# Kernel optimization log

Hardware: AMD Instinct MI355X
Metric: run time of the kernel (lower is better)

## Reference

```python
import jax, jax.numpy as jnp
import numpy as np

B, DS, DM = 4, 64, 4096
NE, S = 1024, 2048


def setup_inputs() -> dict:
    key = jax.random.key(0)
    ks = jax.random.split(key, 9)
    std = 0.02
    return {
        "state": jax.random.normal(ks[0], (B, DS, DM), jnp.float32),
        "evicted_tokens": jax.random.normal(ks[1], (B, NE, DM), jnp.float32),
        "current_tokens": jax.random.normal(ks[2], (B, S, DM), jnp.float32),
        "W_key": std * jax.random.normal(ks[3], (DS, DM), jnp.float32),
        "W_beta_w": std * jax.random.normal(ks[4], (DS, DM), jnp.float32),
        "W_beta_b": jnp.zeros((DS,), jnp.float32),
        "W_query": std * jax.random.normal(ks[5], (DS, DM), jnp.float32),
        "gate_w": std * jax.random.normal(ks[6], (1, DM), jnp.float32),
        "gate_b": jnp.full((1,), -2.0, jnp.float32),  # gate_bias init
    }


def reference(state, evicted_tokens, current_tokens, W_key, W_beta_w, W_beta_b,
              W_query, gate_w, gate_b):
    # ---- compress: fold evicted tokens into SSM state ----
    # keys: [B, NE, DS]; softmax over the token axis (dim=1)
    keys = jnp.einsum('bnd,sd->bns', evicted_tokens, W_key)
    write_weights = jax.nn.softmax(keys, axis=1)
    # update: [B, DS, DM] = write_weights^T @ evicted_tokens
    update = jnp.einsum('bns,bnd->bsd', write_weights, evicted_tokens)
    summary = evicted_tokens.mean(axis=1)  # [B, DM]
    beta = jax.nn.sigmoid(summary @ W_beta_w.T + W_beta_b)  # [B, DS]
    new_state = beta[:, :, None] * state + update  # [B, DS, DM]
    # ---- query: gated linear-attention readout ----
    q = jnp.einsum('bld,sd->bls', current_tokens, W_query)  # [B, S, DS]
    retrieved = jnp.einsum('bls,bsd->bld', q, new_state)    # [B, S, DM]
    gate = jax.nn.sigmoid(current_tokens @ gate_w.T + gate_b)  # [B, S, 1]
    return gate * retrieved
```

## Files before the change

kernel.cpp:

```cpp
#include <hip/hip_runtime.h>

#define DM 4096
#define DSZ 64
#define NE 1024
#define SQ 2048
#define NB 4

typedef __attribute__((ext_vector_type(8))) short bf16x8;
typedef __attribute__((ext_vector_type(4))) float f32x4;

__device__ __forceinline__ unsigned f2bf(float f) {
  union { float f; unsigned u; } v; v.f = f;
  return (v.u + 0x7fffu + ((v.u >> 16) & 1u)) >> 16;
}
__device__ __forceinline__ unsigned pack2(float lo, float hi) {
  return f2bf(lo) | (f2bf(hi) << 16);
}

__launch_bounds__(256)
__global__ void k_keys(const float* __restrict__ ev, const float* __restrict__ Wk,
                       float* __restrict__ keys_part) {
  __shared__ __align__(16) unsigned short As[64][72];
  __shared__ __align__(16) unsigned short Bs[64][72];
  const int bid = blockIdx.x;
  const int ks = bid & 7, mt = (bid >> 3) & 15, b = bid >> 7;
  const int n0 = mt * 64;
  const int t = threadIdx.x;
  const int w = t >> 6, m15 = t & 15, quad = (t & 63) >> 4;
  const int rowS = t >> 2, seg = (t & 3) * 16;

  f32x4 acc[4];
#pragma unroll
  for (int i = 0; i < 4; ++i) acc[i] = (f32x4){0.f, 0.f, 0.f, 0.f};

  const float* ap = ev + ((size_t)(b * NE + n0 + rowS)) * DM + ks * 512 + seg;
  const float* bp = Wk + (size_t)rowS * DM + ks * 512 + seg;

  for (int ch = 0; ch < 8; ++ch) {
    float4 a0 = *(const float4*)(ap);
    float4 a1 = *(const float4*)(ap + 4);
    float4 a2 = *(const float4*)(ap + 8);
    float4 a3 = *(const float4*)(ap + 12);
    float4 b0 = *(const float4*)(bp);
    float4 b1 = *(const float4*)(bp + 4);
    float4 b2 = *(const float4*)(bp + 8);
    float4 b3 = *(const float4*)(bp + 12);
    uint4 pa0 = { pack2(a0.x,a0.y), pack2(a0.z,a0.w), pack2(a1.x,a1.y), pack2(a1.z,a1.w) };
    uint4 pa1 = { pack2(a2.x,a2.y), pack2(a2.z,a2.w), pack2(a3.x,a3.y), pack2(a3.z,a3.w) };
    uint4 pb0 = { pack2(b0.x,b0.y), pack2(b0.z,b0.w), pack2(b1.x,b1.y), pack2(b1.z,b1.w) };
    uint4 pb1 = { pack2(b2.x,b2.y), pack2(b2.z,b2.w), pack2(b3.x,b3.y), pack2(b3.z,b3.w) };
    *(uint4*)&As[rowS][seg]     = pa0;
    *(uint4*)&As[rowS][seg + 8] = pa1;
    *(uint4*)&Bs[rowS][seg]     = pb0;
    *(uint4*)&Bs[rowS][seg + 8] = pb1;
    __syncthreads();
#pragma unroll
    for (int kk = 0; kk < 2; ++kk) {
      bf16x8 af = *(const bf16x8*)&As[w * 16 + m15][kk * 32 + quad * 8];
#pragma unroll
      for (int tn = 0; tn < 4; ++tn) {
        bf16x8 bfr = *(const bf16x8*)&Bs[tn * 16 + m15][kk * 32 + quad * 8];
        acc[tn] = __builtin_amdgcn_mfma_f32_16x16x32_bf16(af, bfr, acc[tn], 0, 0, 0);
      }
    }
    __syncthreads();
    ap += 64; bp += 64;
  }
  const int n = n0 + w * 16 + quad * 4;
#pragma unroll
  for (int tn = 0; tn < 4; ++tn) {
    const int s = tn * 16 + m15;
    float4 v = { acc[tn][0], acc[tn][1], acc[tn][2], acc[tn][3] };
    *(float4*)&keys_part[(size_t)ks * (NB * DSZ * NE) + ((size_t)(b * DSZ + s)) * NE + n] = v;
  }
}

__launch_bounds__(256)
__global__ void k_sum(const float* __restrict__ ev, float* __restrict__ summary) {
  __shared__ float red[256];
  const int bid = blockIdx.x;
  const int b = bid >> 7, rem = bid & 127;
  const int d0 = (rem >> 1) * 64, half = rem & 1;
  const int t = threadIdx.x;
  const int dl = t & 63, g = t >> 6;
  float acc = 0.f;
  const float* p = ev + ((size_t)(b * NE + half * 512 + g * 128)) * DM + d0 + dl;
  for (int i = 0; i < 128; ++i) { acc += *p; p += DM; }
  red[t] = acc;
  __syncthreads();
  if (t < 64) {
    float tot = red[t] + red[t + 64] + red[t + 128] + red[t + 192];
    atomicAdd(&summary[b * DM + d0 + t], tot * (1.f / 1024.f));
  }
}

__launch_bounds__(256)
__global__ void k_beta(const float* __restrict__ summary, const float* __restrict__ Wbw,
                       const float* __restrict__ Wbb, float* __restrict__ beta) {
  __shared__ float red[256];
  const int b = blockIdx.x >> 6, s = blockIdx.x & 63;
  const int t = threadIdx.x;
  const float* sp = summary + b * DM + t * 16;
  const float* wp = Wbw + (size_t)s * DM + t * 16;
  float acc = 0.f;
#pragma unroll
  for (int j = 0; j < 4; ++j) {
    float4 a  = *(const float4*)(sp + j * 4);
    float4 w4 = *(const float4*)(wp + j * 4);
    acc += a.x * w4.x + a.y * w4.y + a.z * w4.z + a.w * w4.w;
  }
  red[t] = acc;
  __syncthreads();
  for (int off = 128; off > 0; off >>= 1) {
    if (t < off) red[t] += red[t + off];
    __syncthreads();
  }
  if (t == 0) {
    float x = red[0] + Wbb[s];
    beta[b * DSZ + s] = 1.f / (1.f + expf(-x));
  }
}

__launch_bounds__(256)
__global__ void k_softmax(const float* __restrict__ keys_part, unsigned short* __restrict__ ww_t) {
  __shared__ float red[256];
  const int b = blockIdx.x >> 6, s = blockIdx.x & 63;
  const int t = threadIdx.x;
  const size_t base = ((size_t)(b * DSZ + s)) * NE + t * 4;
  float4 k = {0.f, 0.f, 0.f, 0.f};
#pragma unroll
  for (int sl = 0; sl < 8; ++sl) {
    float4 p = *(const float4*)&keys_part[(size_t)sl * (NB * DSZ * NE) + base];
    k.x += p.x; k.y += p.y; k.z += p.z; k.w += p.w;
  }
  float m = fmaxf(fmaxf(k.x, k.y), fmaxf(k.z, k.w));
  red[t] = m;
  __syncthreads();
  for (int off = 128; off > 0; off >>= 1) {
    if (t < off) red[t] = fmaxf(red[t], red[t + off]);
    __syncthreads();
  }
  const float M = red[0];
  __syncthreads();
  float4 e = { expf(k.x - M), expf(k.y - M), expf(k.z - M), expf(k.w - M) };
  red[t] = e.x + e.y + e.z + e.w;
  __syncthreads();
  for (int off = 128; off > 0; off >>= 1) {
    if (t < off) red[t] += red[t + off];
    __syncthreads();
  }
  const float inv = 1.f / red[0];
  ushort4 o = { (unsigned short)f2bf(e.x * inv), (unsigned short)f2bf(e.y * inv),
                (unsigned short)f2bf(e.z * inv), (unsigned short)f2bf(e.w * inv) };
  *(ushort4*)&ww_t[((size_t)(b * DSZ + s)) * NE + t * 4] = o;
}

__launch_bounds__(256)
__global__ void k_update(const float* __restrict__ ev, const float* __restrict__ state,
                         const float* __restrict__ beta, const unsigned short* __restrict__ ww_t,
                         unsigned short* __restrict__ ns_t) {
  __shared__ __align__(16) unsigned short Aw[64][72];
  __shared__ __align__(16) unsigned short Bt[64][72];
  const int bid = blockIdx.x;
  const int dt = bid & 63, b = bid >> 6;
  const int d0 = dt * 64;
  const int t = threadIdx.x;
  const int w = t >> 6, m15 = t & 15, quad = (t & 63) >> 4;
  const int rowS = t >> 2, seg = (t & 3) * 16;
  const int npair = (t & 31) * 2, dseg = (t >> 5) * 8;

  f32x4 acc[4];
#pragma unroll
  for (int i = 0; i < 4; ++i) acc[i] = (f32x4){0.f, 0.f, 0.f, 0.f};

  for (int ch = 0; ch < 16; ++ch) {
    const int nch = ch * 64;
    const uint4* wsrc = (const uint4*)&ww_t[((size_t)(b * DSZ + rowS)) * NE + nch + seg];
    uint4 wa = wsrc[0], wb = wsrc[1];
    const float* e0 = ev + ((size_t)(b * NE + nch + npair)) * DM + d0 + dseg;
    const float* e1 = e0 + DM;
    float4 r00 = *(const float4*)(e0);
    float4 r01 = *(const float4*)(e0 + 4);
    float4 r10 = *(const float4*)(e1);
    float4 r11 = *(const float4*)(e1 + 4);
    *(uint4*)&Aw[rowS][seg]     = wa;
    *(uint4*)&Aw[rowS][seg + 8] = wb;
    *(unsigned*)&Bt[dseg + 0][npair] = pack2(r00.x, r10.x);
    *(unsigned*)&Bt[dseg + 1][npair] = pack2(r00.y, r10.y);
    *(unsigned*)&Bt[dseg + 2][npair] = pack2(r00.z, r10.z);
    *(unsigned*)&Bt[dseg + 3][npair] = pack2(r00.w, r10.w);
    *(unsigned*)&Bt[dseg + 4][npair] = pack2(r01.x, r11.x);
    *(unsigned*)&Bt[dseg + 5][npair] = pack2(r01.y, r11.y);
    *(unsigned*)&Bt[dseg + 6][npair] = pack2(r01.z, r11.z);
    *(unsigned*)&Bt[dseg + 7][npair] = pack2(r01.w, r11.w);
    __syncthreads();
#pragma unroll
    for (int kk = 0; kk < 2; ++kk) {
      bf16x8 af = *(const bf16x8*)&Aw[w * 16 + m15][kk * 32 + quad * 8];
#pragma unroll
      for (int tn = 0; tn < 4; ++tn) {
        bf16x8 bfr = *(const bf16x8*)&Bt[tn * 16 + m15][kk * 32 + quad * 8];
        acc[tn] = __builtin_amdgcn_mfma_f32_16x16x32_bf16(af, bfr, acc[tn], 0, 0, 0);
      }
    }
    __syncthreads();
  }
  const int sbase = w * 16 + quad * 4;
#pragma unroll
  for (int tn = 0; tn < 4; ++tn) {
    const int d = d0 + tn * 16 + m15;
    float v[4];
#pragma unroll
    for (int r = 0; r < 4; ++r) {
      const int s = sbase + r;
      v[r] = beta[b * DSZ + s] * state[((size_t)(b * DSZ + s)) * DM + d] + acc[tn][r];
    }
    ushort4 o = { (unsigned short)f2bf(v[0]), (unsigned short)f2bf(v[1]),
                  (unsigned short)f2bf(v[2]), (unsigned short)f2bf(v[3]) };
    *(ushort4*)&ns_t[((size_t)(b * DM + d)) * DSZ + sbase] = o;
  }
}

__launch_bounds__(256)
__global__ void k_q(const float* __restrict__ cur, const float* __restrict__ Wq,
                    const float* __restrict__ gate_w,
                    float* __restrict__ q_part, float* __restrict__ gate_acc) {
  __shared__ __align__(16) unsigned short As[64][72];
  __shared__ __align__(16) unsigned short Bs[64][72];
  __shared__ float gw[64];
  __shared__ float gred[256];
  const int bid = blockIdx.x;
  const int ks = bid & 3, mt = (bid >> 2) & 31, b = bid >> 7;
  const int l0 = mt * 64;
  const int t = threadIdx.x;
  const int w = t >> 6, m15 = t & 15, quad = (t & 63) >> 4;
  const int rowS = t >> 2, seg = (t & 3) * 16;

  f32x4 acc[4];
#pragma unroll
  for (int i = 0; i < 4; ++i) acc[i] = (f32x4){0.f, 0.f, 0.f, 0.f};
  float gpart = 0.f;

  const float* ap = cur + ((size_t)(b * SQ + l0 + rowS)) * DM + ks * 1024 + seg;
  const float* bp = Wq + (size_t)rowS * DM + ks * 1024 + seg;
  const float* gp = gate_w + ks * 1024;

  for (int ch = 0; ch < 16; ++ch) {
    float4 a0 = *(const float4*)(ap);
    float4 a1 = *(const float4*)(ap + 4);
    float4 a2 = *(const float4*)(ap + 8);
    float4 a3 = *(const float4*)(ap + 12);
    float4 b0 = *(const float4*)(bp);
    float4 b1 = *(const float4*)(bp + 4);
    float4 b2 = *(const float4*)(bp + 8);
    float4 b3 = *(const float4*)(bp + 12);
    if (t < 16) *(float4*)&gw[t * 4] = *(const float4*)(gp + ch * 64 + t * 4);
    uint4 pa0 = { pack2(a0.x,a0.y), pack2(a0.z,a0.w), pack2(a1.x,a1.y), pack2(a1.z,a1.w) };
    uint4 pa1 = { pack2(a2.x,a2.y), pack2(a2.z,a2.w), pack2(a3.x,a3.y), pack2(a3.z,a3.w) };
    uint4 pb0 = { pack2(b0.x,b0.y), pack2(b0.z,b0.w), pack2(b1.x,b1.y), pack2(b1.z,b1.w) };
    uint4 pb1 = { pack2(b2.x,b2.y), pack2(b2.z,b2.w), pack2(b3.x,b3.y), pack2(b3.z,b3.w) };
    *(uint4*)&As[rowS][seg]     = pa0;
    *(uint4*)&As[rowS][seg + 8] = pa1;
    *(uint4*)&Bs[rowS][seg]     = pb0;
    *(uint4*)&Bs[rowS][seg + 8] = pb1;
    __syncthreads();
    {
      const float* g = &gw[seg];
      gpart += a0.x*g[0]  + a0.y*g[1]  + a0.z*g[2]  + a0.w*g[3]
             + a1.x*g[4]  + a1.y*g[5]  + a1.z*g[6]  + a1.w*g[7]
             + a2.x*g[8]  + a2.y*g[9]  + a2.z*g[10] + a2.w*g[11]
             + a3.x*g[12] + a3.y*g[13] + a3.z*g[14] + a3.w*g[15];
    }
#pragma unroll
    for (int kk = 0; kk < 2; ++kk) {
      bf16x8 af = *(const bf16x8*)&As[w * 16 + m15][kk * 32 + quad * 8];
#pragma unroll
      for (int tn = 0; tn < 4; ++tn) {
        bf16x8 bfr = *(const bf16x8*)&Bs[tn * 16 + m15][kk * 32 + quad * 8];
        acc[tn] = __builtin_amdgcn_mfma_f32_16x16x32_bf16(af, bfr, acc[tn], 0, 0, 0);
      }
    }
    __syncthreads();
    ap += 64; bp += 64;
  }
  const int lrow = l0 + w * 16 + quad * 4;
#pragma unroll
  for (int tn = 0; tn < 4; ++tn) {
#pragma unroll
    for (int r = 0; r < 4; ++r) {
      q_part[(size_t)ks * (NB * SQ * DSZ) + ((size_t)(b * SQ + lrow + r)) * DSZ + tn * 16 + m15] =
          acc[tn][r];
    }
  }
  gred[t] = gpart;
  __syncthreads();
  if (t < 64) {
    float tot = gred[4 * t] + gred[4 * t + 1] + gred[4 * t + 2] + gred[4 * t + 3];
    atomicAdd(&gate_acc[b * SQ + l0 + t], tot);
  }
}

__launch_bounds__(256)
__global__ void k_qcvt(const float* __restrict__ q_part, unsigned short* __restrict__ qbf) {
  const int i = (blockIdx.x * 256 + threadIdx.x) * 4;
  const int SL = NB * SQ * DSZ;
  float4 v0 = *(const float4*)&q_part[i];
  float4 v1 = *(const float4*)&q_part[i + SL];
  float4 v2 = *(const float4*)&q_part[i + 2 * SL];
  float4 v3 = *(const float4*)&q_part[i + 3 * SL];
  float x = v0.x + v1.x + v2.x + v3.x;
  float y = v0.y + v1.y + v2.y + v3.y;
  float z = v0.z + v1.z + v2.z + v3.z;
  float u = v0.w + v1.w + v2.w + v3.w;
  ushort4 o = { (unsigned short)f2bf(x), (unsigned short)f2bf(y),
                (unsigned short)f2bf(z), (unsigned short)f2bf(u) };
  *(ushort4*)&qbf[i] = o;
}

__launch_bounds__(256)
__global__ void k_out(const unsigned short* __restrict__ qbf, const unsigned short* __restrict__ ns_t,
                      const float* __restrict__ gate_acc, const float* __restrict__ gate_b,
                      float* __restrict__ out) {
  const int bid = blockIdx.x;
  const int dt = bid & 63, lt = (bid >> 6) & 31, b = bid >> 11;
  const int d0 = dt * 64, l0 = lt * 64;
  const int t = threadIdx.x;
  const int w = t >> 6, m15 = t & 15, quad = (t & 63) >> 4;
  const int la = l0 + w * 16 + m15;
  f32x4 acc[4];
#pragma unroll
  for (int i = 0; i < 4; ++i) acc[i] = (f32x4){0.f, 0.f, 0.f, 0.f};
#pragma unroll
  for (int kk = 0; kk < 2; ++kk) {
    bf16x8 af = *(const bf16x8*)&qbf[((size_t)(b * SQ + la)) * DSZ + kk * 32 + quad * 8];
#pragma unroll
    for (int tn = 0; tn < 4; ++tn) {
      const int d = d0 + tn * 16 + m15;
      bf16x8 bfr = *(const bf16x8*)&ns_t[((size_t)(b * DM + d)) * DSZ + kk * 32 + quad * 8];
      acc[tn] = __builtin_amdgcn_mfma_f32_16x16x32_bf16(af, bfr, acc[tn], 0, 0, 0);
    }
  }
  const float gb = gate_b[0];
  const int lbase = l0 + w * 16 + quad * 4;
  float g[4];
#pragma unroll
  for (int r = 0; r < 4; ++r)
    g[r] = 1.f / (1.f + expf(-(gate_acc[b * SQ + lbase + r] + gb)));
#pragma unroll
  for (int tn = 0; tn < 4; ++tn) {
    const int d = d0 + tn * 16 + m15;
#pragma unroll
    for (int r = 0; r < 4; ++r)
      out[((size_t)(b * SQ + lbase + r)) * DM + d] = g[r] * acc[tn][r];
  }
}

extern "C" void kernel_launch(void* const* d_in, const int* in_sizes, int n_in,
                              void* d_out, int out_size, void* d_ws, size_t ws_size,
                              hipStream_t stream) {
  const float* state   = (const float*)d_in[0];
  const float* evicted = (const float*)d_in[1];
  const float* current = (const float*)d_in[2];
  const float* Wkey    = (const float*)d_in[3];
  const float* Wbw     = (const float*)d_in[4];
  const float* Wbb     = (const float*)d_in[5];
  const float* Wq      = (const float*)d_in[6];
  const float* gate_w  = (const float*)d_in[7];
  const float* gate_b  = (const float*)d_in[8];
  float* out = (float*)d_out;

  float* f = (float*)d_ws;
  float* keys_part = f;
  float* q_part    = keys_part + 8 * 262144;
  float* summary   = q_part + 4 * 524288;
  float* gate_acc  = summary + 16384;
  float* beta      = gate_acc + 8192;
  unsigned short* ww_t = (unsigned short*)(beta + 256);
  unsigned short* qbf  = ww_t + 262144;
  unsigned short* ns_t = qbf + 524288;

  hipMemsetAsync(summary, 0, (16384 + 8192) * sizeof(float), stream);

  k_keys   <<<512,  256, 0, stream>>>(evicted, Wkey, keys_part);
  k_sum    <<<512,  256, 0, stream>>>(evicted, summary);
  k_beta   <<<256,  256, 0, stream>>>(summary, Wbw, Wbb, beta);
  k_softmax<<<256,  256, 0, stream>>>(keys_part, ww_t);
  k_update <<<256,  256, 0, stream>>>(evicted, state, beta, ww_t, ns_t);
  k_q      <<<512,  256, 0, stream>>>(current, Wq, gate_w, q_part, gate_acc);
  k_qcvt   <<<512,  256, 0, stream>>>(q_part, qbf);
  k_out    <<<8192, 256, 0, stream>>>(qbf, ns_t, gate_acc, gate_b, out);
}
```

Baseline: 396.5 us.

## Merge independent kernels into fewer launches with register prefetch and split-K reduction fused into k_out

Combines k_keys, k_sum and k_q into one k_front launch dispatched by block index, and k_softmax and k_beta into one k_mid launch. This cuts the launch count from eight to four and lets independent stages share the GPU at the same time. The GEMM loops now prefetch the next chunk into registers while the MFMAs run on the current shared-memory tile. k_update uses 32-wide d tiles to double its block count, and the k_qcvt split-K reduction is folded into k_out. The cost is that each k_out block rereads the four fp32 q partial slices instead of one bf16 buffer.

Result: slower. 419.1 us (+5.7%).

```diff
diff --git a/kernel.cpp b/kernel.cpp
--- a/kernel.cpp
+++ b/kernel.cpp
@@ -17,252 +17,109 @@
   return f2bf(lo) | (f2bf(hi) << 16);
 }
 
+__device__ __forceinline__ void stage16(unsigned short (*S)[72], int row, int seg,
+                                        float4 a0, float4 a1, float4 a2, float4 a3) {
+  uint4 p0 = { pack2(a0.x,a0.y), pack2(a0.z,a0.w), pack2(a1.x,a1.y), pack2(a1.z,a1.w) };
+  uint4 p1 = { pack2(a2.x,a2.y), pack2(a2.z,a2.w), pack2(a3.x,a3.y), pack2(a3.z,a3.w) };
+  *(uint4*)&S[row][seg]     = p0;
+  *(uint4*)&S[row][seg + 8] = p1;
+}
+
+__device__ __forceinline__ void mfma_64x64(const unsigned short (*A)[72], const unsigned short (*B)[72],
+                                           int w, int m15, int quad, f32x4* acc) {
+#pragma unroll
+  for (int kk = 0; kk < 2; ++kk) {
+    bf16x8 af = *(const bf16x8*)&A[w * 16 + m15][kk * 32 + quad * 8];
+#pragma unroll
+    for (int tn = 0; tn < 4; ++tn) {
+      bf16x8 bfr = *(const bf16x8*)&B[tn * 16 + m15][kk * 32 + quad * 8];
+      acc[tn] = __builtin_amdgcn_mfma_f32_16x16x32_bf16(af, bfr, acc[tn], 0, 0, 0);
+    }
+  }
+}
+
 __launch_bounds__(256)
-__global__ void k_keys(const float* __restrict__ ev, const float* __restrict__ Wk,
-                       float* __restrict__ keys_part) {
-  __shared__ __align__(16) unsigned short As[64][72];
-  __shared__ __align__(16) unsigned short Bs[64][72];
-  const int bid = blockIdx.x;
-  const int ks = bid & 7, mt = (bid >> 3) & 15, b = bid >> 7;
-  const int n0 = mt * 64;
-  const int t = threadIdx.x;
-  const int w = t >> 6, m15 = t & 15, quad = (t & 63) >> 4;
-  const int rowS = t >> 2, seg = (t & 3) * 16;
-
-  f32x4 acc[4];
-#pragma unroll
-  for (int i = 0; i < 4; ++i) acc[i] = (f32x4){0.f, 0.f, 0.f, 0.f};
-
-  const float* ap = ev + ((size_t)(b * NE + n0 + rowS)) * DM + ks * 512 + seg;
-  const float* bp = Wk + (size_t)rowS * DM + ks * 512 + seg;
-
-  for (int ch = 0; ch < 8; ++ch) {
-    float4 a0 = *(const float4*)(ap);
-    float4 a1 = *(const float4*)(ap + 4);
-    float4 a2 = *(const float4*)(ap + 8);
-    float4 a3 = *(const float4*)(ap + 12);
-    float4 b0 = *(const float4*)(bp);
-    float4 b1 = *(const float4*)(bp + 4);
-    float4 b2 = *(const float4*)(bp + 8);
-    float4 b3 = *(const float4*)(bp + 12);
-    uint4 pa0 = { pack2(a0.x,a0.y), pack2(a0.z,a0.w), pack2(a1.x,a1.y), pack2(a1.z,a1.w) };
-    uint4 pa1 = { pack2(a2.x,a2.y), pack2(a2.z,a2.w), pack2(a3.x,a3.y), pack2(a3.z,a3.w) };
-    uint4 pb0 = { pack2(b0.x,b0.y), pack2(b0.z,b0.w), pack2(b1.x,b1.y), pack2(b1.z,b1.w) };
-    uint4 pb1 = { pack2(b2.x,b2.y), pack2(b2.z,b2.w), pack2(b3.x,b3.y), pack2(b3.z,b3.w) };
-    *(uint4*)&As[rowS][seg]     = pa0;
-    *(uint4*)&As[rowS][seg + 8] = pa1;
-    *(uint4*)&Bs[rowS][seg]     = pb0;
-    *(uint4*)&Bs[rowS][seg + 8] = pb1;
-    __syncthreads();
-#pragma unroll
-    for (int kk = 0; kk < 2; ++kk) {
-      bf16x8 af = *(const bf16x8*)&As[w * 16 + m15][kk * 32 + quad * 8];
-#pragma unroll
-      for (int tn = 0; tn < 4; ++tn) {
-        bf16x8 bfr = *(const bf16x8*)&Bs[tn * 16 + m15][kk * 32 + quad * 8];
-        acc[tn] = __builtin_amdgcn_mfma_f32_16x16x32_bf16(af, bfr, acc[tn], 0, 0, 0);
-      }
-    }
-    __syncthreads();
-    ap += 64; bp += 64;
-  }
-  const int n = n0 + w * 16 + quad * 4;
-#pragma unroll
-  for (int tn = 0; tn < 4; ++tn) {
-    const int s = tn * 16 + m15;
-    float4 v = { acc[tn][0], acc[tn][1], acc[tn][2], acc[tn][3] };
-    *(float4*)&keys_part[(size_t)ks * (NB * DSZ * NE) + ((size_t)(b * DSZ + s)) * NE + n] = v;
-  }
-}
-
-__launch_bounds__(256)
-__global__ void k_sum(const float* __restrict__ ev, float* __restrict__ summary) {
-  __shared__ float red[256];
-  const int bid = blockIdx.x;
-  const int b = bid >> 7, rem = bid & 127;
-  const int d0 = (rem >> 1) * 64, half = rem & 1;
-  const int t = threadIdx.x;
-  const int dl = t & 63, g = t >> 6;
-  float acc = 0.f;
-  const float* p = ev + ((size_t)(b * NE + half * 512 + g * 128)) * DM + d0 + dl;
-  for (int i = 0; i < 128; ++i) { acc += *p; p += DM; }
-  red[t] = acc;
-  __syncthreads();
-  if (t < 64) {
-    float tot = red[t] + red[t + 64] + red[t + 128] + red[t + 192];
-    atomicAdd(&summary[b * DM + d0 + t], tot * (1.f / 1024.f));
-  }
-}
-
-__launch_bounds__(256)
-__global__ void k_beta(const float* __restrict__ summary, const float* __restrict__ Wbw,
-                       const float* __restrict__ Wbb, float* __restrict__ beta) {
-  __shared__ float red[256];
-  const int b = blockIdx.x >> 6, s = blockIdx.x & 63;
-  const int t = threadIdx.x;
-  const float* sp = summary + b * DM + t * 16;
-  const float* wp = Wbw + (size_t)s * DM + t * 16;
-  float acc = 0.f;
-#pragma unroll
-  for (int j = 0; j < 4; ++j) {
-    float4 a  = *(const float4*)(sp + j * 4);
-    float4 w4 = *(const float4*)(wp + j * 4);
-    acc += a.x * w4.x + a.y * w4.y + a.z * w4.z + a.w * w4.w;
-  }
-  red[t] = acc;
-  __syncthreads();
-  for (int off = 128; off > 0; off >>= 1) {
-    if (t < off) red[t] += red[t + off];
-    __syncthreads();
-  }
-  if (t == 0) {
-    float x = red[0] + Wbb[s];
-    beta[b * DSZ + s] = 1.f / (1.f + expf(-x));
-  }
-}
-
-__launch_bounds__(256)
-__global__ void k_softmax(const float* __restrict__ keys_part, unsigned short* __restrict__ ww_t) {
-  __shared__ float red[256];
-  const int b = blockIdx.x >> 6, s = blockIdx.x & 63;
-  const int t = threadIdx.x;
-  const size_t base = ((size_t)(b * DSZ + s)) * NE + t * 4;
-  float4 k = {0.f, 0.f, 0.f, 0.f};
-#pragma unroll
-  for (int sl = 0; sl < 8; ++sl) {
-    float4 p = *(const float4*)&keys_part[(size_t)sl * (NB * DSZ * NE) + base];
-    k.x += p.x; k.y += p.y; k.z += p.z; k.w += p.w;
-  }
-  float m = fmaxf(fmaxf(k.x, k.y), fmaxf(k.z, k.w));
-  red[t] = m;
-  __syncthreads();
-  for (int off = 128; off > 0; off >>= 1) {
-    if (t < off) red[t] = fmaxf(red[t], red[t + off]);
-    __syncthreads();
-  }
-  const float M = red[0];
-  __syncthreads();
-  float4 e = { expf(k.x - M), expf(k.y - M), expf(k.z - M), expf(k.w - M) };
-  red[t] = e.x + e.y + e.z + e.w;
-  __syncthreads();
-  for (int off = 128; off > 0; off >>= 1) {
-    if (t < off) red[t] += red[t + off];
-    __syncthreads();
-  }
-  const float inv = 1.f / red[0];
-  ushort4 o = { (unsigned short)f2bf(e.x * inv), (unsigned short)f2bf(e.y * inv),
-                (unsigned short)f2bf(e.z * inv), (unsigned short)f2bf(e.w * inv) };
-  *(ushort4*)&ww_t[((size_t)(b * DSZ + s)) * NE + t * 4] = o;
-}
-
-__launch_bounds__(256)
-__global__ void k_update(const float* __restrict__ ev, const float* __restrict__ state,
-                         const float* __restrict__ beta, const unsigned short* __restrict__ ww_t,
-                         unsigned short* __restrict__ ns_t) {
-  __shared__ __align__(16) unsigned short Aw[64][72];
-  __shared__ __align__(16) unsigned short Bt[64][72];
-  const int bid = blockIdx.x;
-  const int dt = bid & 63, b = bid >> 6;
-  const int d0 = dt * 64;
-  const int t = threadIdx.x;
-  const int w = t >> 6, m15 = t & 15, quad = (t & 63) >> 4;
-  const int rowS = t >> 2, seg = (t & 3) * 16;
-  const int npair = (t & 31) * 2, dseg = (t >> 5) * 8;
-
-  f32x4 acc[4];
-#pragma unroll
-  for (int i = 0; i < 4; ++i) acc[i] = (f32x4){0.f, 0.f, 0.f, 0.f};
-
-  for (int ch = 0; ch < 16; ++ch) {
-    const int nch = ch * 64;
-    const uint4* wsrc = (const uint4*)&ww_t[((size_t)(b * DSZ + rowS)) * NE + nch + seg];
-    uint4 wa = wsrc[0], wb = wsrc[1];
-    const float* e0 = ev + ((size_t)(b * NE + nch + npair)) * DM + d0 + dseg;
-    const float* e1 = e0 + DM;
-    float4 r00 = *(const float4*)(e0);
-    float4 r01 = *(const float4*)(e0 + 4);
-    float4 r10 = *(const float4*)(e1);
-    float4 r11 = *(const float4*)(e1 + 4);
-    *(uint4*)&Aw[rowS][seg]     = wa;
-    *(uint4*)&Aw[rowS][seg + 8] = wb;
-    *(unsigned*)&Bt[dseg + 0][npair] = pack2(r00.x, r10.x);
-    *(unsigned*)&Bt[dseg + 1][npair] = pack2(r00.y, r10.y);
-    *(unsigned*)&Bt[dseg + 2][npair] = pack2(r00.z, r10.z);
-    *(unsigned*)&Bt[dseg + 3][npair] = pack2(r00.w, r10.w);
-    *(unsigned*)&Bt[dseg + 4][npair] = pack2(r01.x, r11.x);
-    *(unsigned*)&Bt[dseg + 5][npair] = pack2(r01.y, r11.y);
-    *(unsigned*)&Bt[dseg + 6][npair] = pack2(r01.z, r11.z);
-    *(unsigned*)&Bt[dseg + 7][npair] = pack2(r01.w, r11.w);
-    __syncthreads();
-#pragma unroll
-    for (int kk = 0; kk < 2; ++kk) {
-      bf16x8 af = *(const bf16x8*)&Aw[w * 16 + m15][kk * 32 + quad * 8];
-#pragma unroll
-      for (int tn = 0; tn < 4; ++tn) {
-        bf16x8 bfr = *(const bf16x8*)&Bt[tn * 16 + m15][kk * 32 + quad * 8];
-        acc[tn] = __builtin_amdgcn_mfma_f32_16x16x32_bf16(af, bfr, acc[tn], 0, 0, 0);
-      }
-    }
-    __syncthreads();
-  }
-  const int sbase = w * 16 + quad * 4;
-#pragma unroll
-  for (int tn = 0; tn < 4; ++tn) {
-    const int d = d0 + tn * 16 + m15;
-    float v[4];
-#pragma unroll
-    for (int r = 0; r < 4; ++r) {
-      const int s = sbase + r;
-      v[r] = beta[b * DSZ + s] * state[((size_t)(b * DSZ + s)) * DM + d] + acc[tn][r];
-    }
-    ushort4 o = { (unsigned short)f2bf(v[0]), (unsigned short)f2bf(v[1]),
-                  (unsigned short)f2bf(v[2]), (unsigned short)f2bf(v[3]) };
-    *(ushort4*)&ns_t[((size_t)(b * DM + d)) * DSZ + sbase] = o;
-  }
-}
-
-__launch_bounds__(256)
-__global__ void k_q(const float* __restrict__ cur, const float* __restrict__ Wq,
-                    const float* __restrict__ gate_w,
-                    float* __restrict__ q_part, float* __restrict__ gate_acc) {
+__global__ void k_front(const float* __restrict__ ev, const float* __restrict__ Wk,
+                        const float* __restrict__ cur, const float* __restrict__ Wq,
+                        const float* __restrict__ gate_w,
+                        float* __restrict__ keys_part, float* __restrict__ q_part,
+                        float* __restrict__ summary, float* __restrict__ gate_acc) {
   __shared__ __align__(16) unsigned short As[64][72];
   __shared__ __align__(16) unsigned short Bs[64][72];
   __shared__ float gw[64];
   __shared__ float gred[256];
   const int bid = blockIdx.x;
-  const int ks = bid & 3, mt = (bid >> 2) & 31, b = bid >> 7;
-  const int l0 = mt * 64;
   const int t = threadIdx.x;
+
+  if (bid >= 512 && bid < 1024) {
+    const int bid2 = bid - 512;
+    const int b = bid2 >> 7, rem = bid2 & 127;
+    const int d0 = (rem >> 1) * 64, half = rem & 1;
+    const int dl = t & 63, g = t >> 6;
+    float acc = 0.f;
+    const float* p = ev + ((size_t)(b * NE + half * 512 + g * 128)) * DM + d0 + dl;
+    for (int i = 0; i < 128; ++i) { acc += *p; p += DM; }
+    gred[t] = acc;
+    __syncthreads();
+    if (t < 64) {
+      float tot = gred[t] + gred[t + 64] + gred[t + 128] + gred[t + 192];
+      atomicAdd(&summary[b * DM + d0 + t], tot * (1.f / 1024.f));
+    }
+    return;
+  }
+
   const int w = t >> 6, m15 = t & 15, quad = (t & 63) >> 4;
   const int rowS = t >> 2, seg = (t & 3) * 16;
-
   f32x4 acc[4];
 #pragma unroll
   for (int i = 0; i < 4; ++i) acc[i] = (f32x4){0.f, 0.f, 0.f, 0.f};
+
+  if (bid < 512) {
+    const int ks = bid & 7, mt = (bid >> 3) & 15, b = bid >> 7;
+    const int n0 = mt * 64;
+    const float* ap0 = ev + ((size_t)(b * NE + n0 + rowS)) * DM + ks * 512 + seg;
+    const float* bp0 = Wk + (size_t)rowS * DM + ks * 512 + seg;
+    float4 a0 = *(const float4*)(ap0),     a1 = *(const float4*)(ap0 + 4);
+    float4 a2 = *(const float4*)(ap0 + 8), a3 = *(const float4*)(ap0 + 12);
+    float4 b0 = *(const float4*)(bp0),     b1 = *(const float4*)(bp0 + 4);
+    float4 b2 = *(const float4*)(bp0 + 8), b3 = *(const float4*)(bp0 + 12);
+    for (int ch = 0; ch < 8; ++ch) {
+      stage16(As, rowS, seg, a0, a1, a2, a3);
+      stage16(Bs, rowS, seg, b0, b1, b2, b3);
+      __syncthreads();
+      const int off = (ch < 7 ? ch + 1 : 7) * 64;
+      a0 = *(const float4*)(ap0 + off);      a1 = *(const float4*)(ap0 + off + 4);
+      a2 = *(const float4*)(ap0 + off + 8);  a3 = *(const float4*)(ap0 + off + 12);
+      b0 = *(const float4*)(bp0 + off);      b1 = *(const float4*)(bp0 + off + 4);
+      b2 = *(const float4*)(bp0 + off + 8);  b3 = *(const float4*)(bp0 + off + 12);
+      mfma_64x64(As, Bs, w, m15, quad, acc);
+      __syncthreads();
+    }
+    const int n = n0 + w * 16 + quad * 4;
+#pragma unroll
+    for (int tn = 0; tn < 4; ++tn) {
+      const int s = tn * 16 + m15;
+      float4 v = { acc[tn][0], acc[tn][1], acc[tn][2], acc[tn][3] };
+      *(float4*)&keys_part[(size_t)ks * (NB * DSZ * NE) + ((size_t)(b * DSZ + s)) * NE + n] = v;
+    }
+    return;
+  }
+
+  const int bid2 = bid - 1024;
+  const int ks = bid2 & 3, mt = (bid2 >> 2) & 31, b = bid2 >> 7;
+  const int l0 = mt * 64;
   float gpart = 0.f;
-
-  const float* ap = cur + ((size_t)(b * SQ + l0 + rowS)) * DM + ks * 1024 + seg;
-  const float* bp = Wq + (size_t)rowS * DM + ks * 1024 + seg;
+  const float* ap0 = cur + ((size_t)(b * SQ + l0 + rowS)) * DM + ks * 1024 + seg;
+  const float* bp0 = Wq + (size_t)rowS * DM + ks * 1024 + seg;
   const float* gp = gate_w + ks * 1024;
-
+  float4 a0 = *(const float4*)(ap0),     a1 = *(const float4*)(ap0 + 4);
+  float4 a2 = *(const float4*)(ap0 + 8), a3 = *(const float4*)(ap0 + 12);
+  float4 b0 = *(const float4*)(bp0),     b1 = *(const float4*)(bp0 + 4);
+  float4 b2 = *(const float4*)(bp0 + 8), b3 = *(const float4*)(bp0 + 12);
   for (int ch = 0; ch < 16; ++ch) {
-    float4 a0 = *(const float4*)(ap);
-    float4 a1 = *(const float4*)(ap + 4);
-    float4 a2 = *(const float4*)(ap + 8);
-    float4 a3 = *(const float4*)(ap + 12);
-    float4 b0 = *(const float4*)(bp);
-    float4 b1 = *(const float4*)(bp + 4);
-    float4 b2 = *(const float4*)(bp + 8);
-    float4 b3 = *(const float4*)(bp + 12);
+    stage16(As, rowS, seg, a0, a1, a2, a3);
+    stage16(Bs, rowS, seg, b0, b1, b2, b3);
     if (t < 16) *(float4*)&gw[t * 4] = *(const float4*)(gp + ch * 64 + t * 4);
-    uint4 pa0 = { pack2(a0.x,a0.y), pack2(a0.z,a0.w), pack2(a1.x,a1.y), pack2(a1.z,a1.w) };
-    uint4 pa1 = { pack2(a2.x,a2.y), pack2(a2.z,a2.w), pack2(a3.x,a3.y), pack2(a3.z,a3.w) };
-    uint4 pb0 = { pack2(b0.x,b0.y), pack2(b0.z,b0.w), pack2(b1.x,b1.y), pack2(b1.z,b1.w) };
-    uint4 pb1 = { pack2(b2.x,b2.y), pack2(b2.z,b2.w), pack2(b3.x,b3.y), pack2(b3.z,b3.w) };
-    *(uint4*)&As[rowS][seg]     = pa0;
-    *(uint4*)&As[rowS][seg + 8] = pa1;
-    *(uint4*)&Bs[rowS][seg]     = pb0;
-    *(uint4*)&Bs[rowS][seg + 8] = pb1;
     __syncthreads();
     {
       const float* g = &gw[seg];
@@ -271,17 +128,13 @@
              + a2.x*g[8]  + a2.y*g[9]  + a2.z*g[10] + a2.w*g[11]
              + a3.x*g[12] + a3.y*g[13] + a3.z*g[14] + a3.w*g[15];
     }
-#pragma unroll
-    for (int kk = 0; kk < 2; ++kk) {
-      bf16x8 af = *(const bf16x8*)&As[w * 16 + m15][kk * 32 + quad * 8];
-#pragma unroll
-      for (int tn = 0; tn < 4; ++tn) {
-        bf16x8 bfr = *(const bf16x8*)&Bs[tn * 16 + m15][kk * 32 + quad * 8];
-        acc[tn] = __builtin_amdgcn_mfma_f32_16x16x32_bf16(af, bfr, acc[tn], 0, 0, 0);
-      }
-    }
-    __syncthreads();
-    ap += 64; bp += 64;
+    const int off = (ch < 15 ? ch + 1 : 15) * 64;
+    a0 = *(const float4*)(ap0 + off);      a1 = *(const float4*)(ap0 + off + 4);
+    a2 = *(const float4*)(ap0 + off + 8);  a3 = *(const float4*)(ap0 + off + 12);
+    b0 = *(const float4*)(bp0 + off);      b1 = *(const float4*)(bp0 + off + 4);
+    b2 = *(const float4*)(bp0 + off + 8);  b3 = *(const float4*)(bp0 + off + 12);
+    mfma_64x64(As, Bs, w, m15, quad, acc);
+    __syncthreads();
   }
   const int lrow = l0 + w * 16 + quad * 4;
 #pragma unroll
@@ -301,24 +154,131 @@
 }
 
 __launch_bounds__(256)
-__global__ void k_qcvt(const float* __restrict__ q_part, unsigned short* __restrict__ qbf) {
-  const int i = (blockIdx.x * 256 + threadIdx.x) * 4;
-  const int SL = NB * SQ * DSZ;
-  float4 v0 = *(const float4*)&q_part[i];
-  float4 v1 = *(const float4*)&q_part[i + SL];
-  float4 v2 = *(const float4*)&q_part[i + 2 * SL];
-  float4 v3 = *(const float4*)&q_part[i + 3 * SL];
-  float x = v0.x + v1.x + v2.x + v3.x;
-  float y = v0.y + v1.y + v2.y + v3.y;
-  float z = v0.z + v1.z + v2.z + v3.z;
-  float u = v0.w + v1.w + v2.w + v3.w;
-  ushort4 o = { (unsigned short)f2bf(x), (unsigned short)f2bf(y),
-                (unsigned short)f2bf(z), (unsigned short)f2bf(u) };
-  *(ushort4*)&qbf[i] = o;
+__global__ void k_mid(const float* __restrict__ keys_part, const float* __restrict__ summary,
+                      const float* __restrict__ Wbw, const float* __restrict__ Wbb,
+                      float* __restrict__ beta, unsigned short* __restrict__ ww_t) {
+  __shared__ float red[256];
+  const int t = threadIdx.x;
+  if (blockIdx.x < 256) {
+    const int b = blockIdx.x >> 6, s = blockIdx.x & 63;
+    const size_t base = ((size_t)(b * DSZ + s)) * NE + t * 4;
+    float4 k = {0.f, 0.f, 0.f, 0.f};
+#pragma unroll
+    for (int sl = 0; sl < 8; ++sl) {
+      float4 p = *(const float4*)&keys_part[(size_t)sl * (NB * DSZ * NE) + base];
+      k.x += p.x; k.y += p.y; k.z += p.z; k.w += p.w;
+    }
+    float m = fmaxf(fmaxf(k.x, k.y), fmaxf(k.z, k.w));
+    red[t] = m;
+    __syncthreads();
+    for (int off = 128; off > 0; off >>= 1) {
+      if (t < off) red[t] = fmaxf(red[t], red[t + off]);
+      __syncthreads();
+    }
+    const float M = red[0];
+    __syncthreads();
+    float4 e = { expf(k.x - M), expf(k.y - M), expf(k.z - M), expf(k.w - M) };
+    red[t] = e.x + e.y + e.z + e.w;
+    __syncthreads();
+    for (int off = 128; off > 0; off >>= 1) {
+      if (t < off) red[t] += red[t + off];
+      __syncthreads();
+    }
+    const float inv = 1.f / red[0];
+    ushort4 o = { (unsigned short)f2bf(e.x * inv), (unsigned short)f2bf(e.y * inv),
+                  (unsigned short)f2bf(e.z * inv), (unsigned short)f2bf(e.w * inv) };
+    *(ushort4*)&ww_t[((size_t)(b * DSZ + s)) * NE + t * 4] = o;
+  } else {
+    const int bx = blockIdx.x - 256;
+    const int b = bx >> 6, s = bx & 63;
+    const float* sp = summary + b * DM + t * 16;
+    const float* wp = Wbw + (size_t)s * DM + t * 16;
+    float acc = 0.f;
+#pragma unroll
+    for (int j = 0; j < 4; ++j) {
+      float4 a  = *(const float4*)(sp + j * 4);
+      float4 w4 = *(const float4*)(wp + j * 4);
+      acc += a.x * w4.x + a.y * w4.y + a.z * w4.z + a.w * w4.w;
+    }
+    red[t] = acc;
+    __syncthreads();
+    for (int off = 128; off > 0; off >>= 1) {
+      if (t < off) red[t] += red[t + off];
+      __syncthreads();
+    }
+    if (t == 0) {
+      float x = red[0] + Wbb[s];
+      beta[b * DSZ + s] = 1.f / (1.f + expf(-x));
+    }
+  }
 }
 
 __launch_bounds__(256)
-__global__ void k_out(const unsigned short* __restrict__ qbf, const unsigned short* __restrict__ ns_t,
+__global__ void k_update(const float* __restrict__ ev, const float* __restrict__ state,
+                         const float* __restrict__ beta, const unsigned short* __restrict__ ww_t,
+                         unsigned short* __restrict__ ns_t) {
+  __shared__ __align__(16) unsigned short Aw[64][72];
+  __shared__ __align__(16) unsigned short Bt[32][72];
+  const int bid = blockIdx.x;
+  const int dt = bid & 127, b = bid >> 7;
+  const int d0 = dt * 32;
+  const int t = threadIdx.x;
+  const int w = t >> 6, m15 = t & 15, quad = (t & 63) >> 4;
+  const int rowS = t >> 2, seg = (t & 3) * 16;
+  const int npair = (t & 31) * 2, dquad = (t >> 5) * 4;
+
+  f32x4 acc[2];
+  acc[0] = (f32x4){0.f, 0.f, 0.f, 0.f};
+  acc[1] = (f32x4){0.f, 0.f, 0.f, 0.f};
+
+  const unsigned short* wp0 = ww_t + ((size_t)(b * DSZ + rowS)) * NE + seg;
+  const float* ep0 = ev + ((size_t)(b * NE + npair)) * DM + d0 + dquad;
+  uint4 wa = *(const uint4*)(wp0), wb = *(const uint4*)(wp0 + 8);
+  float4 r0 = *(const float4*)(ep0), r1 = *(const float4*)(ep0 + DM);
+
+  for (int ch = 0; ch < 16; ++ch) {
+    *(uint4*)&Aw[rowS][seg]     = wa;
+    *(uint4*)&Aw[rowS][seg + 8] = wb;
+    *(unsigned*)&Bt[dquad + 0][npair] = pack2(r0.x, r1.x);
+    *(unsigned*)&Bt[dquad + 1][npair] = pack2(r0.y, r1.y);
+    *(unsigned*)&Bt[dquad + 2][npair] = pack2(r0.z, r1.z);
+    *(unsigned*)&Bt[dquad + 3][npair] = pack2(r0.w, r1.w);
+    __syncthreads();
+    const int nn = (ch < 15 ? ch + 1 : 15) * 64;
+    wa = *(const uint4*)(wp0 + nn);
+    wb = *(const uint4*)(wp0 + nn + 8);
+    const float* epn = ep0 + (size_t)nn * DM;
+    r0 = *(const float4*)(epn);
+    r1 = *(const float4*)(epn + DM);
+#pragma unroll
+    for (int kk = 0; kk < 2; ++kk) {
+      bf16x8 af = *(const bf16x8*)&Aw[w * 16 + m15][kk * 32 + quad * 8];
+#pragma unroll
+      for (int tn = 0; tn < 2; ++tn) {
+        bf16x8 bfr = *(const bf16x8*)&Bt[tn * 16 + m15][kk * 32 + quad * 8];
+        acc[tn] = __builtin_amdgcn_mfma_f32_16x16x32_bf16(af, bfr, acc[tn], 0, 0, 0);
+      }
+    }
+    __syncthreads();
+  }
+  const int sbase = w * 16 + quad * 4;
+#pragma unroll
+  for (int tn = 0; tn < 2; ++tn) {
+    const int d = d0 + tn * 16 + m15;
+    float v[4];
+#pragma unroll
+    for (int r = 0; r < 4; ++r) {
+      const int s = sbase + r;
+      v[r] = beta[b * DSZ + s] * state[((size_t)(b * DSZ + s)) * DM + d] + acc[tn][r];
+    }
+    ushort4 o = { (unsigned short)f2bf(v[0]), (unsigned short)f2bf(v[1]),
+                  (unsigned short)f2bf(v[2]), (unsigned short)f2bf(v[3]) };
+    *(ushort4*)&ns_t[((size_t)(b * DM + d)) * DSZ + sbase] = o;
+  }
+}
+
+__launch_bounds__(256)
+__global__ void k_out(const float* __restrict__ q_part, const unsigned short* __restrict__ ns_t,
                       const float* __restrict__ gate_acc, const float* __restrict__ gate_b,
                       float* __restrict__ out) {
   const int bid = blockIdx.x;
@@ -327,17 +287,30 @@
   const int t = threadIdx.x;
   const int w = t >> 6, m15 = t & 15, quad = (t & 63) >> 4;
   const int la = l0 + w * 16 + m15;
+  const int SL = NB * SQ * DSZ;
   f32x4 acc[4];
 #pragma unroll
   for (int i = 0; i < 4; ++i) acc[i] = (f32x4){0.f, 0.f, 0.f, 0.f};
 #pragma unroll
   for (int kk = 0; kk < 2; ++kk) {
-    bf16x8 af = *(const bf16x8*)&qbf[((size_t)(b * SQ + la)) * DSZ + kk * 32 + quad * 8];
+    const size_t qi = ((size_t)(b * SQ + la)) * DSZ + kk * 32 + quad * 8;
+    float4 s0 = *(const float4*)&q_part[qi];
+    float4 s1 = *(const float4*)&q_part[qi + 4];
+#pragma unroll
+    for (int sl = 1; sl < 4; ++sl) {
+      float4 u0 = *(const float4*)&q_part[(size_t)sl * SL + qi];
+      float4 u1 = *(const float4*)&q_part[(size_t)sl * SL + qi + 4];
+      s0.x += u0.x; s0.y += u0.y; s0.z += u0.z; s0.w += u0.w;
+      s1.x += u1.x; s1.y += u1.y; s1.z += u1.z; s1.w += u1.w;
+    }
+    union { bf16x8 v; unsigned u[4]; } af;
+    af.u[0] = pack2(s0.x, s0.y); af.u[1] = pack2(s0.z, s0.w);
+    af.u[2] = pack2(s1.x, s1.y); af.u[3] = pack2(s1.z, s1.w);
 #pragma unroll
     for (int tn = 0; tn < 4; ++tn) {
       const int d = d0 + tn * 16 + m15;
       bf16x8 bfr = *(const bf16x8*)&ns_t[((size_t)(b * DM + d)) * DSZ + kk * 32 + quad * 8];
-      acc[tn] = __builtin_amdgcn_mfma_f32_16x16x32_bf16(af, bfr, acc[tn], 0, 0, 0);
+      acc[tn] = __builtin_amdgcn_mfma_f32_16x16x32_bf16(af.v, bfr, acc[tn], 0, 0, 0);
     }
   }
   const float gb = gate_b[0];
@@ -376,17 +349,13 @@
   float* gate_acc  = summary + 16384;
   float* beta      = gate_acc + 8192;
   unsigned short* ww_t = (unsigned short*)(beta + 256);
-  unsigned short* qbf  = ww_t + 262144;
-  unsigned short* ns_t = qbf + 524288;
+  unsigned short* ns_t = ww_t + 262144;
 
   hipMemsetAsync(summary, 0, (16384 + 8192) * sizeof(float), stream);
 
-  k_keys   <<<512,  256, 0, stream>>>(evicted, Wkey, keys_part);
-  k_sum    <<<512,  256, 0, stream>>>(evicted, summary);
-  k_beta   <<<256,  256, 0, stream>>>(summary, Wbw, Wbb, beta);
-  k_softmax<<<256,  256, 0, stream>>>(keys_part, ww_t);
-  k_update <<<256,  256, 0, stream>>>(evicted, state, beta, ww_t, ns_t);
-  k_q      <<<512,  256, 0, stream>>>(current, Wq, gate_w, q_part, gate_acc);
-  k_qcvt   <<<512,  256, 0, stream>>>(q_part, qbf);
-  k_out    <<<8192, 256, 0, stream>>>(qbf, ns_t, gate_acc, gate_b, out);
-}
+  k_front <<<1536, 256, 0, stream>>>(evicted, Wkey, current, Wq, gate_w,
+                                     keys_part, q_part, summary, gate_acc);
+  k_mid   <<<512,  256, 0, stream>>>(keys_part, summary, Wbw, Wbb, beta, ww_t);
+  k_update<<<512,  256, 0, stream>>>(evicted, state, beta, ww_t, ns_t);
+  k_out   <<<8192, 256, 0, stream>>>(q_part, ns_t, gate_acc, gate_b, out);
+}
```
